# Optimization experiments

Measured on AMD Instinct MI355X. Metric: run time of the kernel, lower is better.

The kernel has to match this reference:

```python
import jax, jax.numpy as jnp
import numpy as np

H, C = 4, 128            # heads, per-head channels (GATConv(in, 128, heads=4))
HC = H * C               # 512
NEG_SLOPE = 0.2          # PyG GATConv default LeakyReLU slope
EPS_BN = 1e-5


def gat_conv(x, src, dst, W, a_src, a_dst, b, n_nodes):
    # x: [N, F_in], W: [F_in, H*C], a_src/a_dst: [H, C], b: [H*C]
    h = (x @ W).reshape(n_nodes, H, C)                       # [N,H,C]
    al_s = jnp.einsum('nhc,hc->nh', h, a_src)                # [N,H]
    al_d = jnp.einsum('nhc,hc->nh', h, a_dst)                # [N,H]
    e = jax.nn.leaky_relu(al_s[src] + al_d[dst], NEG_SLOPE)  # [E,H] per-edge logits
    m = jax.ops.segment_max(e, dst, num_segments=n_nodes)    # stable segment softmax
    p = jnp.exp(e - m[dst])
    s = jax.ops.segment_sum(p, dst, num_segments=n_nodes)
    alpha = p / (s[dst] + 1e-16)                             # [E,H]
    out = jax.ops.segment_sum(h[src] * alpha[:, :, None], dst, num_segments=n_nodes)
    return out.reshape(n_nodes, HC) + b                      # concat heads + bias


def batch_norm(x, g, b):
    mu = x.mean(0)
    var = x.var(0)  # biased, as torch BatchNorm1d uses for normalization
    return (x - mu) * jax.lax.rsqrt(var + EPS_BN) * g + b


def setup_inputs() -> dict:
    N, E, F_IN, OUT = 20000, 256000, 128, 10
    key = jax.random.key(0)
    ks = jax.random.split(key, 40)
    sc = 0.05
    inp = {
        'x': jax.random.normal(ks[0], (N, F_IN), dtype=jnp.float32),
        'edge_index': jax.random.randint(ks[1], (2, E), 0, N, dtype=jnp.int64) if jax.config.jax_enable_x64 else jax.random.randint(ks[1], (2, E), 0, N).astype(jnp.int32),
        'batch': jnp.zeros((N,), dtype=jnp.int32),
    }
    k = 2
    fin = F_IN
    for i in range(1, 5):
        inp[f'W{i}'] = jax.random.normal(ks[k], (fin, HC), dtype=jnp.float32) * sc; k += 1
        inp[f'as{i}'] = jax.random.normal(ks[k], (H, C), dtype=jnp.float32) * sc; k += 1
        inp[f'ad{i}'] = jax.random.normal(ks[k], (H, C), dtype=jnp.float32) * sc; k += 1
        inp[f'b{i}'] = jnp.zeros((HC,), dtype=jnp.float32)
        inp[f'g{i}'] = jnp.ones((HC,), dtype=jnp.float32)
        inp[f'bt{i}'] = jnp.zeros((HC,), dtype=jnp.float32)
        fin = HC
    inp['lw1'] = jax.random.normal(ks[k], (HC, 128), dtype=jnp.float32) * sc; k += 1
    inp['lb1'] = jnp.zeros((128,), dtype=jnp.float32)
    inp['lw2'] = jax.random.normal(ks[k], (128, 64), dtype=jnp.float32) * sc; k += 1
    inp['lb2'] = jnp.zeros((64,), dtype=jnp.float32)
    inp['lw3'] = jax.random.normal(ks[k], (64, OUT), dtype=jnp.float32) * sc; k += 1
    inp['lb3'] = jnp.zeros((OUT,), dtype=jnp.float32)
    return inp


def reference(x, edge_index, batch,
              W1, as1, ad1, b1, g1, bt1,
              W2, as2, ad2, b2, g2, bt2,
              W3, as3, ad3, b3, g3, bt3,
              W4, as4, ad4, b4, g4, bt4,
              lw1, lb1, lw2, lb2, lw3, lb3):
    n = x.shape[0]
    # add self-loops (PyG GATConv default add_self_loops=True)
    loops = jnp.arange(n, dtype=edge_index.dtype)
    src = jnp.concatenate([edge_index[0], loops])
    dst = jnp.concatenate([edge_index[1], loops])

    h = jax.nn.elu(gat_conv(x, src, dst, W1, as1, ad1, b1, n))
    h = batch_norm(h, g1, bt1)
    h = jax.nn.elu(gat_conv(h, src, dst, W2, as2, ad2, b2, n))
    h = batch_norm(h, g2, bt2)
    h = jax.nn.elu(gat_conv(h, src, dst, W3, as3, ad3, b3, n))
    h = batch_norm(h, g3, bt3)
    h = jax.nn.elu(gat_conv(h, src, dst, W4, as4, ad4, b4, n))
    h = batch_norm(h, g4, bt4)

    h = jax.nn.relu(h @ lw1 + lb1)   # dropout is identity in eval
    h = jax.nn.relu(h @ lw2 + lb2)
    return jax.nn.log_softmax(h @ lw3 + lb3, axis=-1)
```

## Files before the change

kernel.cpp:

```cpp
#include <hip/hip_runtime.h>
#include <hip/hip_bf16.h>
#include <math.h>

#define HC 512
#define NHEAD 4
#define NEG_SLOPE 0.2f
#define EPS_BN 1e-5f

typedef __attribute__((ext_vector_type(8))) _Float16 half8;
typedef __attribute__((ext_vector_type(4))) _Float16 half4v;
typedef __attribute__((ext_vector_type(2))) _Float16 half2v;
typedef __attribute__((ext_vector_type(4))) float f32x4;

#define GLOAD16(gptr, lptr)                                                      \
    __builtin_amdgcn_global_load_lds(                                            \
        (const __attribute__((address_space(1))) unsigned int*)(gptr),           \
        (__attribute__((address_space(3))) unsigned int*)(lptr), 16, 0, 0)

__global__ void hist_kernel(const int* __restrict__ dstE, int* __restrict__ cnt,
                            int E, int N) {
    int i = blockIdx.x * 256 + threadIdx.x;
    if (i < E + N) {
        int d = (i < E) ? dstE[i] : (i - E);
        atomicAdd(&cnt[d], 1);
    }
}

__global__ __launch_bounds__(1024) void scan_kernel(int* __restrict__ rowptr,
                                                    int* __restrict__ wr, int n) {
    __shared__ int wsum[16];
    __shared__ int carry_s;
    int t = threadIdx.x, lane = t & 63, wv = t >> 6;
    if (t == 0) carry_s = 0;
    __syncthreads();
    for (int base = 0; base < n; base += 1024) {
        int v = (base + t < n) ? rowptr[base + t] : 0;
        int x = v;
#pragma unroll
        for (int off = 1; off < 64; off <<= 1) {
            int y = __shfl_up(x, off);
            if (lane >= off) x += y;
        }
        if (lane == 63) wsum[wv] = x;
        __syncthreads();
        if (wv == 0) {
            int s = (lane < 16) ? wsum[lane] : 0;
#pragma unroll
            for (int off = 1; off < 16; off <<= 1) {
                int y = __shfl_up(s, off);
                if (lane >= off) s += y;
            }
            if (lane < 16) wsum[lane] = s;
        }
        __syncthreads();
        int woff = (wv == 0) ? 0 : wsum[wv - 1];
        int tot = wsum[15];
        int carry = carry_s;
        if (base + t < n) {
            int excl = carry + woff + x - v;
            rowptr[base + t] = excl;
            wr[base + t] = excl;
        }
        __syncthreads();
        if (t == 1023) carry_s = carry + tot;
        __syncthreads();
    }
    if (threadIdx.x == 0) rowptr[n] = carry_s;
}

__global__ void scatter_kernel(const int* __restrict__ srcE,
                               const int* __restrict__ dstE,
                               int* __restrict__ wr, int* __restrict__ csrc,
                               int E, int N) {
    int i = blockIdx.x * 256 + threadIdx.x;
    if (i < E + N) {
        int d = (i < E) ? dstE[i] : (i - E);
        int s = (i < E) ? srcE[i] : (i - E);
        int p = atomicAdd(&wr[d], 1);
        csrc[p] = s;
    }
}

__global__ __launch_bounds__(256) void advec_kernel(const double* __restrict__ stats,
                                                    const float* __restrict__ g,
                                                    const float* __restrict__ bt,
                                                    float* __restrict__ avec,
                                                    float* __restrict__ dvec,
                                                    double invN) {
    int k = blockIdx.x * 256 + threadIdx.x;
    if (k >= HC) return;
    double mu = stats[k] * invN;
    double var = stats[HC + k] * invN - mu * mu;
    float a = g[k] * (float)rsqrt(var + (double)EPS_BN);
    avec[k] = a;
    dvec[k] = bt[k] - (float)mu * a;
}

__global__ __launch_bounds__(256) void wsplit_kernel(const float* __restrict__ W,
                                                     const float* __restrict__ avec,
                                                     _Float16* __restrict__ hiT,
                                                     _Float16* __restrict__ loT,
                                                     int K, int Nc) {
    __shared__ float tile[32][33];
    int bx = blockIdx.x * 32;
    int by = blockIdx.y * 32;
    int tx = threadIdx.x & 31, ty = threadIdx.x >> 5;
#pragma unroll
    for (int r = 0; r < 32; r += 8)
        tile[ty + r][tx] = W[(size_t)(by + ty + r) * Nc + bx + tx];
    __syncthreads();
    int k = by + tx;
    float a = avec ? avec[k] : 1.f;
#pragma unroll
    for (int r = 0; r < 32; r += 8) {
        int n = bx + ty + r;
        float w = tile[tx][ty + r] * a;
        _Float16 h = (_Float16)w;
        hiT[(size_t)n * K + k] = h;
        loT[(size_t)n * K + k] = (_Float16)(w - (float)h);
    }
}

__global__ __launch_bounds__(256) void bvec_kernel(const float* __restrict__ W,
                                                   const float* __restrict__ dvec,
                                                   const float* __restrict__ extra,
                                                   float* __restrict__ bvec,
                                                   int K, int Nc) {
    int wv = (blockIdx.x * 256 + threadIdx.x) >> 6;
    int lane = threadIdx.x & 63;
    if (wv >= Nc) return;
    float s = 0.f;
    for (int k = lane; k < K; k += 64)
        s = fmaf(dvec[k], W[(size_t)k * Nc + wv], s);
#pragma unroll
    for (int off = 32; off; off >>= 1) s += __shfl_xor(s, off);
    if (lane == 0) bvec[wv] = s + (extra ? extra[wv] : 0.f);
}

__global__ __launch_bounds__(256) void xcvt_kernel(const float* __restrict__ x,
                                                   _Float16* __restrict__ xh, int total) {
    for (int i = blockIdx.x * 256 + threadIdx.x; i < total; i += gridDim.x * 256)
        xh[i] = (_Float16)x[i];
}

template <int EPI>
__global__ __launch_bounds__(256) void mfma_gemm(const _Float16* __restrict__ A,
                                                 const _Float16* __restrict__ BThi,
                                                 const _Float16* __restrict__ BTlo,
                                                 const float* __restrict__ bvec,
                                                 _Float16* __restrict__ H16,
                                                 float* __restrict__ C,
                                                 int M, int K, int Nc) {
    __shared__ _Float16 sm[3 * 4096];
    _Float16* sA  = sm;
    _Float16* sBh = sm + 4096;
    _Float16* sBl = sm + 8192;

    const int nwg = gridDim.x * gridDim.y;
    const int orig = blockIdx.y * gridDim.x + blockIdx.x;
    const int q = nwg >> 3, r = nwg & 7;
    const int xcd = orig & 7, local = orig >> 3;
    const int wgid = (xcd < r ? xcd * (q + 1) : r * (q + 1) + (xcd - r) * q) + local;
    const int bxi = wgid % gridDim.x, byi = wgid / gridDim.x;

    const int tid = threadIdx.x;
    const int wid = tid >> 6, lane = tid & 63;
    const int wm = wid >> 1, wn = wid & 1;
    const int bm = byi * 128, bn = bxi * 128;

    const int rowl = lane >> 2;
    const int cole = (lane & 3) * 8;
    const int c0 = wid * 2;

    const int frow = lane & 15;
    const int fko = (lane >> 4) * 8;

    f32x4 acc[4][4] = {};

    for (int k0 = 0; k0 < K; k0 += 32) {
#pragma unroll
        for (int cc = 0; cc < 2; ++cc) {
            int c = c0 + cc;
            int ra = bm + c * 16 + rowl; if (ra >= M) ra = M - 1;
            int rb = bn + c * 16 + rowl;
            GLOAD16(A + (size_t)ra * K + k0 + cole, &sA[c * 512]);
            GLOAD16(BThi + (size_t)rb * K + k0 + cole, &sBh[c * 512]);
            GLOAD16(BTlo + (size_t)rb * K + k0 + cole, &sBl[c * 512]);
        }
        __syncthreads();

        half8 av[4], bh[4], bl[4];
#pragma unroll
        for (int mi = 0; mi < 4; ++mi) {
            int rr = wm * 64 + mi * 16 + frow;
            av[mi] = *(const half8*)&sA[rr * 32 + fko];
        }
#pragma unroll
        for (int ni = 0; ni < 4; ++ni) {
            int rr = wn * 64 + ni * 16 + frow;
            bh[ni] = *(const half8*)&sBh[rr * 32 + fko];
            bl[ni] = *(const half8*)&sBl[rr * 32 + fko];
        }
#pragma unroll
        for (int mi = 0; mi < 4; ++mi)
#pragma unroll
            for (int ni = 0; ni < 4; ++ni) {
                acc[mi][ni] = __builtin_amdgcn_mfma_f32_16x16x32_f16(av[mi], bh[ni], acc[mi][ni], 0, 0, 0);
                acc[mi][ni] = __builtin_amdgcn_mfma_f32_16x16x32_f16(av[mi], bl[ni], acc[mi][ni], 0, 0, 0);
            }
        __syncthreads();
    }

    const int crow = (lane >> 4) * 4;
    const int ccol = lane & 15;
#pragma unroll
    for (int mi = 0; mi < 4; ++mi)
#pragma unroll
        for (int ni = 0; ni < 4; ++ni) {
            int gc = bn + wn * 64 + ni * 16 + ccol;
            float bv = bvec[gc];
#pragma unroll
            for (int rr = 0; rr < 4; ++rr) {
                int gr = bm + wm * 64 + mi * 16 + crow + rr;
                if (gr >= M) continue;
                float v = acc[mi][ni][rr] + bv;
                if (EPI == 0) {
                    H16[(size_t)gr * Nc + gc] = (_Float16)v;
                } else {
                    C[(size_t)gr * Nc + gc] = fmaxf(v, 0.f);
                }
            }
        }
}

template <int BM, int BN, int BK, int TM, int TN, int EPI>
__global__ __launch_bounds__(256) void gemm_k(const float* __restrict__ A,
                                              const float* __restrict__ B,
                                              const float* __restrict__ bias,
                                              float* __restrict__ C,
                                              int M, int K, int N) {
    constexpr int PAD = 4;
    __shared__ float sA[BK][BM + PAD];
    __shared__ float sB[BK][BN];

    const int tid = threadIdx.x;
    const int bm = blockIdx.y * BM, bn = blockIdx.x * BN;
    constexpr int TX = BN / TN;
    const int tx = tid % TX, ty = tid / TX;

    float acc[TM][TN] = {};

    constexpr int AF4 = BK / 4;
    const int a4 = tid % AF4;
    const int ar0 = tid / AF4;
    constexpr int AROWS = 256 / AF4;
    constexpr int APASS = BM / AROWS;

    constexpr int BF4 = BN / 4;
    const int b4 = tid % BF4;
    const int br0 = tid / BF4;
    constexpr int BROWS = 256 / BF4;
    constexpr int BPASS = BK / BROWS;

    for (int kt = 0; kt < K; kt += BK) {
        __syncthreads();
#pragma unroll
        for (int p = 0; p < APASS; ++p) {
            int row = ar0 + p * AROWS;
            int gr = bm + row;
            if (gr >= M) gr = M - 1;
            float4 v = *(const float4*)&A[(size_t)gr * K + kt + a4 * 4];
            sA[a4 * 4 + 0][row] = v.x;
            sA[a4 * 4 + 1][row] = v.y;
            sA[a4 * 4 + 2][row] = v.z;
            sA[a4 * 4 + 3][row] = v.w;
        }
#pragma unroll
        for (int p = 0; p < BPASS; ++p) {
            int row = br0 + p * BROWS;
            float4 v = *(const float4*)&B[(size_t)(kt + row) * N + bn + b4 * 4];
            *(float4*)&sB[row][b4 * 4] = v;
        }
        __syncthreads();
#pragma unroll
        for (int k = 0; k < BK; ++k) {
            float ar[TM], br[TN];
#pragma unroll
            for (int i = 0; i < TM; i += 4)
                *(float4*)&ar[i] = *(const float4*)&sA[k][ty * TM + i];
#pragma unroll
            for (int j = 0; j < TN; j += 4)
                *(float4*)&br[j] = *(const float4*)&sB[k][tx * TN + j];
#pragma unroll
            for (int i = 0; i < TM; ++i)
#pragma unroll
                for (int j = 0; j < TN; ++j)
                    acc[i][j] = fmaf(ar[i], br[j], acc[i][j]);
        }
    }

#pragma unroll
    for (int i = 0; i < TM; ++i) {
        int r = bm + ty * TM + i;
        if (r >= M) continue;
#pragma unroll
        for (int j = 0; j < TN; j += 4) {
            int c = bn + tx * TN + j;
            float4 v;
            v.x = acc[i][j + 0]; v.y = acc[i][j + 1];
            v.z = acc[i][j + 2]; v.w = acc[i][j + 3];
            if (EPI == 1) {
                v.x = fmaxf(v.x + bias[c + 0], 0.f);
                v.y = fmaxf(v.y + bias[c + 1], 0.f);
                v.z = fmaxf(v.z + bias[c + 2], 0.f);
                v.w = fmaxf(v.w + bias[c + 3], 0.f);
            }
            *(float4*)&C[(size_t)r * N + c] = v;
        }
    }
}

__global__ __launch_bounds__(256) void al_kernel(const _Float16* __restrict__ h16,
                                                 const float* __restrict__ asrc,
                                                 const float* __restrict__ adst,
                                                 float* __restrict__ al_s,
                                                 float* __restrict__ al_d, int N) {
    int wid = (blockIdx.x * 256 + threadIdx.x) >> 6;
    int lane = threadIdx.x & 63;
    if (wid >= N) return;
    half8 hv = *(const half8*)(h16 + (size_t)wid * HC + lane * 8);
    float ss = 0.f, sd = 0.f;
#pragma unroll
    for (int j = 0; j < 8; ++j) {
        float v = (float)hv[j];
        ss = fmaf(v, asrc[lane * 8 + j], ss);
        sd = fmaf(v, adst[lane * 8 + j], sd);
    }
#pragma unroll
    for (int off = 8; off; off >>= 1) {
        ss += __shfl_xor(ss, off);
        sd += __shfl_xor(sd, off);
    }
    if ((lane & 15) == 0) {
        al_s[wid * NHEAD + (lane >> 4)] = ss;
        al_d[wid * NHEAD + (lane >> 4)] = sd;
    }
}

__global__ __launch_bounds__(256) void attw_kernel(const float* __restrict__ al_s,
                                                   const float* __restrict__ al_d,
                                                   const int* __restrict__ rowptr,
                                                   const int* __restrict__ csrc,
                                                   float4* __restrict__ alpha, int N) {
    int node = (blockIdx.x * 256 + threadIdx.x) >> 6;
    int lane = threadIdx.x & 63;
    if (node >= N) return;
    int e0 = rowptr[node], e1 = rowptr[node + 1];
    int deg = e1 - e0;
    float4 ad4 = *(const float4*)&al_d[node * NHEAD];

    if (deg <= 64) {
        float x0 = -INFINITY, x1 = -INFINITY, x2 = -INFINITY, x3 = -INFINITY;
        if (lane < deg) {
            int s = csrc[e0 + lane];
            float4 a = *(const float4*)&al_s[s * NHEAD];
            x0 = a.x + ad4.x; x0 = (x0 > 0.f) ? x0 : NEG_SLOPE * x0;
            x1 = a.y + ad4.y; x1 = (x1 > 0.f) ? x1 : NEG_SLOPE * x1;
            x2 = a.z + ad4.z; x2 = (x2 > 0.f) ? x2 : NEG_SLOPE * x2;
            x3 = a.w + ad4.w; x3 = (x3 > 0.f) ? x3 : NEG_SLOPE * x3;
        }
        float m0 = x0, m1 = x1, m2 = x2, m3 = x3;
#pragma unroll
        for (int off = 32; off; off >>= 1) {
            m0 = fmaxf(m0, __shfl_xor(m0, off));
            m1 = fmaxf(m1, __shfl_xor(m1, off));
            m2 = fmaxf(m2, __shfl_xor(m2, off));
            m3 = fmaxf(m3, __shfl_xor(m3, off));
        }
        float p0 = (lane < deg) ? __expf(x0 - m0) : 0.f;
        float p1 = (lane < deg) ? __expf(x1 - m1) : 0.f;
        float p2 = (lane < deg) ? __expf(x2 - m2) : 0.f;
        float p3 = (lane < deg) ? __expf(x3 - m3) : 0.f;
        float s0 = p0, s1 = p1, s2 = p2, s3 = p3;
#pragma unroll
        for (int off = 32; off; off >>= 1) {
            s0 += __shfl_xor(s0, off);
            s1 += __shfl_xor(s1, off);
            s2 += __shfl_xor(s2, off);
            s3 += __shfl_xor(s3, off);
        }
        if (lane < deg) {
            float4 w;
            w.x = p0 / (s0 + 1e-16f);
            w.y = p1 / (s1 + 1e-16f);
            w.z = p2 / (s2 + 1e-16f);
            w.w = p3 / (s3 + 1e-16f);
            alpha[e0 + lane] = w;
        }
        return;
    }

    float m0 = -INFINITY, m1 = -INFINITY, m2 = -INFINITY, m3 = -INFINITY;
    for (int i = e0 + lane; i < e1; i += 64) {
        int s = csrc[i];
        float4 a = *(const float4*)&al_s[s * NHEAD];
        float e;
        e = a.x + ad4.x; e = (e > 0.f) ? e : NEG_SLOPE * e; m0 = fmaxf(m0, e);
        e = a.y + ad4.y; e = (e > 0.f) ? e : NEG_SLOPE * e; m1 = fmaxf(m1, e);
        e = a.z + ad4.z; e = (e > 0.f) ? e : NEG_SLOPE * e; m2 = fmaxf(m2, e);
        e = a.w + ad4.w; e = (e > 0.f) ? e : NEG_SLOPE * e; m3 = fmaxf(m3, e);
    }
#pragma unroll
    for (int off = 32; off; off >>= 1) {
        m0 = fmaxf(m0, __shfl_xor(m0, off));
        m1 = fmaxf(m1, __shfl_xor(m1, off));
        m2 = fmaxf(m2, __shfl_xor(m2, off));
        m3 = fmaxf(m3, __shfl_xor(m3, off));
    }
    float s0 = 0, s1 = 0, s2 = 0, s3 = 0;
    for (int i = e0 + lane; i < e1; i += 64) {
        int s = csrc[i];
        float4 a = *(const float4*)&al_s[s * NHEAD];
        float e;
        e = a.x + ad4.x; e = (e > 0.f) ? e : NEG_SLOPE * e; s0 += __expf(e - m0);
        e = a.y + ad4.y; e = (e > 0.f) ? e : NEG_SLOPE * e; s1 += __expf(e - m1);
        e = a.z + ad4.z; e = (e > 0.f) ? e : NEG_SLOPE * e; s2 += __expf(e - m2);
        e = a.w + ad4.w; e = (e > 0.f) ? e : NEG_SLOPE * e; s3 += __expf(e - m3);
    }
#pragma unroll
    for (int off = 32; off; off >>= 1) {
        s0 += __shfl_xor(s0, off);
        s1 += __shfl_xor(s1, off);
        s2 += __shfl_xor(s2, off);
        s3 += __shfl_xor(s3, off);
    }
    float r0 = 1.f / (s0 + 1e-16f), r1 = 1.f / (s1 + 1e-16f);
    float r2 = 1.f / (s2 + 1e-16f), r3 = 1.f / (s3 + 1e-16f);
    for (int i = e0 + lane; i < e1; i += 64) {
        int s = csrc[i];
        float4 a = *(const float4*)&al_s[s * NHEAD];
        float4 w;
        float e;
        e = a.x + ad4.x; e = (e > 0.f) ? e : NEG_SLOPE * e; w.x = __expf(e - m0) * r0;
        e = a.y + ad4.y; e = (e > 0.f) ? e : NEG_SLOPE * e; w.y = __expf(e - m1) * r1;
        e = a.z + ad4.z; e = (e > 0.f) ? e : NEG_SLOPE * e; w.z = __expf(e - m2) * r2;
        e = a.w + ad4.w; e = (e > 0.f) ? e : NEG_SLOPE * e; w.w = __expf(e - m3) * r3;
        alpha[i] = w;
    }
}

__global__ __launch_bounds__(256) void gath_kernel(const _Float16* __restrict__ h16,
                                                   const float4* __restrict__ alpha,
                                                   const int* __restrict__ rowptr,
                                                   const int* __restrict__ csrc,
                                                   const float* __restrict__ bias,
                                                   _Float16* __restrict__ out16, int N) {
    int gid = blockIdx.x * 256 + threadIdx.x;
    int wv = gid >> 6, lane = gid & 63;
    int node = wv >> 1, hf = wv & 1;
    if (node >= N) return;
    int e0 = rowptr[node], e1 = rowptr[node + 1];
    size_t cb = (size_t)(hf * 256 + lane * 4);
    bool hiHead = (lane & 32) != 0;

#define PICKW(q) (hf ? (hiHead ? (q).w : (q).z) : (hiHead ? (q).y : (q).x))

    float a0 = 0, a1 = 0, a2 = 0, a3 = 0;
    int i = e0;
    for (; i + 4 <= e1; i += 4) {
        int s0 = csrc[i], s1 = csrc[i + 1], s2 = csrc[i + 2], s3 = csrc[i + 3];
        float4 q0 = alpha[i], q1 = alpha[i + 1], q2 = alpha[i + 2], q3 = alpha[i + 3];
        half4v v0 = *(const half4v*)(h16 + (size_t)s0 * HC + cb);
        half4v v1 = *(const half4v*)(h16 + (size_t)s1 * HC + cb);
        half4v v2 = *(const half4v*)(h16 + (size_t)s2 * HC + cb);
        half4v v3 = *(const half4v*)(h16 + (size_t)s3 * HC + cb);
        float w0 = PICKW(q0), w1 = PICKW(q1), w2 = PICKW(q2), w3 = PICKW(q3);
        a0 = fmaf((float)v0[0], w0, a0); a1 = fmaf((float)v0[1], w0, a1);
        a2 = fmaf((float)v0[2], w0, a2); a3 = fmaf((float)v0[3], w0, a3);
        a0 = fmaf((float)v1[0], w1, a0); a1 = fmaf((float)v1[1], w1, a1);
        a2 = fmaf((float)v1[2], w1, a2); a3 = fmaf((float)v1[3], w1, a3);
        a0 = fmaf((float)v2[0], w2, a0); a1 = fmaf((float)v2[1], w2, a1);
        a2 = fmaf((float)v2[2], w2, a2); a3 = fmaf((float)v2[3], w2, a3);
        a0 = fmaf((float)v3[0], w3, a0); a1 = fmaf((float)v3[1], w3, a1);
        a2 = fmaf((float)v3[2], w3, a2); a3 = fmaf((float)v3[3], w3, a3);
    }
    for (; i < e1; ++i) {
        int s = csrc[i];
        float4 q = alpha[i];
        float w = PICKW(q);
        half4v v = *(const half4v*)(h16 + (size_t)s * HC + cb);
        a0 = fmaf((float)v[0], w, a0); a1 = fmaf((float)v[1], w, a1);
        a2 = fmaf((float)v[2], w, a2); a3 = fmaf((float)v[3], w, a3);
    }
#undef PICKW

    float4 bb = *(const float4*)&bias[cb];
    a0 += bb.x; a1 += bb.y; a2 += bb.z; a3 += bb.w;
    a0 = (a0 > 0.f) ? a0 : (__expf(a0) - 1.f);
    a1 = (a1 > 0.f) ? a1 : (__expf(a1) - 1.f);
    a2 = (a2 > 0.f) ? a2 : (__expf(a2) - 1.f);
    a3 = (a3 > 0.f) ? a3 : (__expf(a3) - 1.f);
    half4v o = {(_Float16)a0, (_Float16)a1, (_Float16)a2, (_Float16)a3};
    *(half4v*)(out16 + (size_t)node * HC + cb) = o;
}

__global__ __launch_bounds__(256) void bnstat_kernel(const _Float16* __restrict__ x,
                                                     double* __restrict__ partials,
                                                     int N) {
    __shared__ double lds[2][4][HC];
    int t = threadIdx.x;
    int lane = t & 63, wv = t >> 6;
    int c0 = lane * 8;
    const int stride = gridDim.x * 4;

    float s[8] = {}, q[8] = {};
    int r = blockIdx.x * 4 + wv;
    for (; r + stride < N; r += 2 * stride) {
        half8 v0 = *(const half8*)&x[(size_t)r * HC + c0];
        half8 v1 = *(const half8*)&x[(size_t)(r + stride) * HC + c0];
#pragma unroll
        for (int j = 0; j < 8; ++j) {
            float f0 = (float)v0[j], f1 = (float)v1[j];
            s[j] += f0 + f1;
            q[j] = fmaf(f0, f0, q[j]);
            q[j] = fmaf(f1, f1, q[j]);
        }
    }
    for (; r < N; r += stride) {
        half8 v0 = *(const half8*)&x[(size_t)r * HC + c0];
#pragma unroll
        for (int j = 0; j < 8; ++j) {
            float f0 = (float)v0[j];
            s[j] += f0;
            q[j] = fmaf(f0, f0, q[j]);
        }
    }
#pragma unroll
    for (int j = 0; j < 8; ++j) {
        lds[0][wv][c0 + j] = (double)s[j];
        lds[1][wv][c0 + j] = (double)q[j];
    }
    __syncthreads();
    if (wv == 0) {
        double* pb = partials + (size_t)blockIdx.x * 1024;
#pragma unroll
        for (int j = 0; j < 8; ++j) {
            int c = c0 + j;
            double ds = lds[0][0][c] + lds[0][1][c] + lds[0][2][c] + lds[0][3][c];
            double dq = lds[1][0][c] + lds[1][1][c] + lds[1][2][c] + lds[1][3][c];
            pb[c] = ds;
            pb[512 + c] = dq;
        }
    }
}

__global__ __launch_bounds__(256) void bnred_kernel(const double* __restrict__ partials,
                                                    double* __restrict__ stats, int nb) {
    int wv = (blockIdx.x * 256 + threadIdx.x) >> 6;
    int lane = threadIdx.x & 63;
    if (wv >= 1024) return;
    double s = 0.0;
    for (int b = lane; b < nb; b += 64)
        s += partials[(size_t)b * 1024 + wv];
#pragma unroll
    for (int off = 32; off; off >>= 1) s += __shfl_xor(s, off);
    if (lane == 0) stats[wv] = s;
}

__global__ __launch_bounds__(256) void head_kernel(const float* __restrict__ x,
                                                   const float* __restrict__ w,
                                                   const float* __restrict__ b,
                                                   float* __restrict__ out, int N) {
    int wid = (blockIdx.x * 256 + threadIdx.x) >> 6;
    int lane = threadIdx.x & 63;
    if (wid >= N) return;
    float v = x[(size_t)wid * 64 + lane];
    float my = -INFINITY;
#pragma unroll
    for (int j = 0; j < 10; ++j) {
        float t = v * w[lane * 10 + j];
#pragma unroll
        for (int off = 32; off; off >>= 1) t += __shfl_xor(t, off);
        t += b[j];
        if (lane == j) my = t;
    }
    float mx = my;
#pragma unroll
    for (int off = 32; off; off >>= 1) mx = fmaxf(mx, __shfl_xor(mx, off));
    float p = (lane < 10) ? expf(my - mx) : 0.f;
    float sum = p;
#pragma unroll
    for (int off = 32; off; off >>= 1) sum += __shfl_xor(sum, off);
    if (lane < 10) out[(size_t)wid * 10 + lane] = my - mx - logf(sum);
}

extern "C" void kernel_launch(void* const* d_in, const int* in_sizes, int n_in,
                              void* d_out, int out_size, void* d_ws, size_t ws_size,
                              hipStream_t stream) {
    const float* x = (const float*)d_in[0];
    const int* ei = (const int*)d_in[1];
    const int N = in_sizes[0] / 128;
    const int E = in_sizes[1] / 2;
    const int EN = E + N;
    const int NB_STAT = 256;

    double* stats = (double*)d_ws;
    double* partials = stats + 1024;
    float* als   = (float*)(partials + (size_t)NB_STAT * 1024);
    float* ald   = als + (size_t)N * NHEAD;
    float4* alpha = (float4*)(ald + (size_t)N * NHEAD);
    float* bvec  = (float*)(alpha + EN);
    float* avec  = bvec + 512;
    float* dvec  = avec + 512;
    float* m1    = dvec + 512;
    float* m2    = m1 + (size_t)N * 128;
    _Float16* xh   = (_Float16*)(m2 + (size_t)N * 64);
    _Float16* h16  = xh + (size_t)N * 128;
    _Float16* out16 = h16 + (size_t)N * HC;
    _Float16* wpool = out16 + (size_t)N * HC;
    _Float16* wthi[4], * wtlo[4], * wtmhi, * wtmlo;
    {
        _Float16* p = wpool;
        wthi[0] = p; p += 512 * 128;
        wtlo[0] = p; p += 512 * 128;
        for (int L = 1; L < 4; ++L) {
            wthi[L] = p; p += 512 * 512;
            wtlo[L] = p; p += 512 * 512;
        }
        wtmhi = p; p += 128 * 512;
        wtmlo = p; p += 128 * 512;
    }
    int* rowptr = (int*)(wpool + 2 * 512 * 128 + 6 * 512 * 512 + 2 * 128 * 512);
    int* wr = rowptr + (N + 1);
    int* csrc = wr + N;

    hipMemsetAsync(rowptr, 0, (N + 1) * sizeof(int), stream);
    hist_kernel<<<(EN + 255) / 256, 256, 0, stream>>>(ei + E, rowptr, E, N);
    scan_kernel<<<1, 1024, 0, stream>>>(rowptr, wr, N);
    scatter_kernel<<<(EN + 255) / 256, 256, 0, stream>>>(ei, ei + E, wr, csrc, E, N);

    wsplit_kernel<<<dim3(512 / 32, 128 / 32), 256, 0, stream>>>(
        (const float*)d_in[3], nullptr, wthi[0], wtlo[0], 128, 512);
    xcvt_kernel<<<1024, 256, 0, stream>>>(x, xh, N * 128);
    hipMemsetAsync(bvec, 0, 512 * sizeof(float), stream);

    const int nodeBlocks = (N * 64 + 255) / 256;
    const int gathBlocks = (N * 128 + 255) / 256;
    const double invN = 1.0 / (double)N;

    for (int L = 0; L < 4; ++L) {
        const float* as_ = (const float*)d_in[4 + 6 * L];
        const float* ad_ = (const float*)d_in[5 + 6 * L];
        const float* b_  = (const float*)d_in[6 + 6 * L];
        const float* g_  = (const float*)d_in[7 + 6 * L];
        const float* bt_ = (const float*)d_in[8 + 6 * L];
        const _Float16* Ain = (L == 0) ? xh : out16;
        const int curK = (L == 0) ? 128 : 512;

        mfma_gemm<0><<<dim3(HC / 128, (N + 127) / 128), 256, 0, stream>>>(
            Ain, wthi[L], wtlo[L], bvec, h16, nullptr, N, curK, HC);
        al_kernel<<<nodeBlocks, 256, 0, stream>>>(h16, as_, ad_, als, ald, N);
        attw_kernel<<<nodeBlocks, 256, 0, stream>>>(als, ald, rowptr, csrc, alpha, N);
        gath_kernel<<<gathBlocks, 256, 0, stream>>>(h16, alpha, rowptr, csrc, b_,
                                                    out16, N);
        bnstat_kernel<<<NB_STAT, 256, 0, stream>>>(out16, partials, N);
        bnred_kernel<<<256, 256, 0, stream>>>(partials, stats, NB_STAT);
        advec_kernel<<<2, 256, 0, stream>>>(stats, g_, bt_, avec, dvec, invN);

        if (L < 3) {
            const float* Wn = (const float*)d_in[3 + 6 * (L + 1)];
            wsplit_kernel<<<dim3(512 / 32, 512 / 32), 256, 0, stream>>>(
                Wn, avec, wthi[L + 1], wtlo[L + 1], 512, 512);
            bvec_kernel<<<(512 * 64 + 255) / 256, 256, 0, stream>>>(
                Wn, dvec, nullptr, bvec, 512, 512);
        } else {
            const float* lw1 = (const float*)d_in[27];
            const float* lb1 = (const float*)d_in[28];
            wsplit_kernel<<<dim3(128 / 32, 512 / 32), 256, 0, stream>>>(
                lw1, avec, wtmhi, wtmlo, 512, 128);
            bvec_kernel<<<(128 * 64 + 255) / 256, 256, 0, stream>>>(
                lw1, dvec, lb1, bvec, 512, 128);
        }
    }

    const float* lw2 = (const float*)d_in[29];
    const float* lb2 = (const float*)d_in[30];
    const float* lw3 = (const float*)d_in[31];
    const float* lb3 = (const float*)d_in[32];

    mfma_gemm<1><<<dim3(1, (N + 127) / 128), 256, 0, stream>>>(
        out16, wtmhi, wtmlo, bvec, nullptr, m1, N, 512, 128);
    gemm_k<64, 64, 16, 4, 4, 1><<<dim3(1, (N + 63) / 64), 256, 0, stream>>>(
        m1, lw2, lb2, m2, N, 128, 64);
    head_kernel<<<nodeBlocks, 256, 0, stream>>>(m2, lw3, lb3, (float*)d_out, N);
}
```

Measured before the change: 680.1 us.

## Drop split-fp16 weight correction and pad CSR rows to multiples of eight

Weights are now converted to a single fp16 copy instead of a hi/lo pair, which halves the MFMA count and the B-tile LDS traffic in every GEMM. Separately, each CSR row is padded to a multiple of eight using zeroed alpha and zeroed source indices. This lets the gather loop run a fixed 8-wide unrolled batch of loads with no remainder loop. The cost is lower weight precision, plus extra memsets and padded edges that gather node 0's features with zero weight.

Result: no change. 685.8 us (+0.8%).

```diff
diff --git a/kernel.cpp b/kernel.cpp
--- a/kernel.cpp
+++ b/kernel.cpp
@@ -9,7 +9,6 @@
 
 typedef __attribute__((ext_vector_type(8))) _Float16 half8;
 typedef __attribute__((ext_vector_type(4))) _Float16 half4v;
-typedef __attribute__((ext_vector_type(2))) _Float16 half2v;
 typedef __attribute__((ext_vector_type(4))) float f32x4;
 
 #define GLOAD16(gptr, lptr)                                                      \
@@ -27,14 +26,16 @@
 }
 
 __global__ __launch_bounds__(1024) void scan_kernel(int* __restrict__ rowptr,
-                                                    int* __restrict__ wr, int n) {
+                                                    int* __restrict__ wr,
+                                                    int* __restrict__ deg, int n) {
     __shared__ int wsum[16];
     __shared__ int carry_s;
     int t = threadIdx.x, lane = t & 63, wv = t >> 6;
     if (t == 0) carry_s = 0;
     __syncthreads();
     for (int base = 0; base < n; base += 1024) {
-        int v = (base + t < n) ? rowptr[base + t] : 0;
+        int c = (base + t < n) ? rowptr[base + t] : 0;
+        int v = (c + 7) & ~7;
         int x = v;
 #pragma unroll
         for (int off = 1; off < 64; off <<= 1) {
@@ -60,6 +61,7 @@
             int excl = carry + woff + x - v;
             rowptr[base + t] = excl;
             wr[base + t] = excl;
+            deg[base + t] = c;
         }
         __syncthreads();
         if (t == 1023) carry_s = carry + tot;
@@ -99,7 +101,6 @@
 __global__ __launch_bounds__(256) void wsplit_kernel(const float* __restrict__ W,
                                                      const float* __restrict__ avec,
                                                      _Float16* __restrict__ hiT,
-                                                     _Float16* __restrict__ loT,
                                                      int K, int Nc) {
     __shared__ float tile[32][33];
     int bx = blockIdx.x * 32;
@@ -114,10 +115,7 @@
 #pragma unroll
     for (int r = 0; r < 32; r += 8) {
         int n = bx + ty + r;
-        float w = tile[tx][ty + r] * a;
-        _Float16 h = (_Float16)w;
-        hiT[(size_t)n * K + k] = h;
-        loT[(size_t)n * K + k] = (_Float16)(w - (float)h);
+        hiT[(size_t)n * K + k] = (_Float16)(tile[tx][ty + r] * a);
     }
 }
 
@@ -145,16 +143,14 @@
 
 template <int EPI>
 __global__ __launch_bounds__(256) void mfma_gemm(const _Float16* __restrict__ A,
-                                                 const _Float16* __restrict__ BThi,
-                                                 const _Float16* __restrict__ BTlo,
+                                                 const _Float16* __restrict__ BT,
                                                  const float* __restrict__ bvec,
                                                  _Float16* __restrict__ H16,
                                                  float* __restrict__ C,
                                                  int M, int K, int Nc) {
-    __shared__ _Float16 sm[3 * 4096];
-    _Float16* sA  = sm;
-    _Float16* sBh = sm + 4096;
-    _Float16* sBl = sm + 8192;
+    __shared__ _Float16 sm[2 * 4096];
+    _Float16* sA = sm;
+    _Float16* sB = sm + 4096;
 
     const int nwg = gridDim.x * gridDim.y;
     const int orig = blockIdx.y * gridDim.x + blockIdx.x;
@@ -184,12 +180,11 @@
             int ra = bm + c * 16 + rowl; if (ra >= M) ra = M - 1;
             int rb = bn + c * 16 + rowl;
             GLOAD16(A + (size_t)ra * K + k0 + cole, &sA[c * 512]);
-            GLOAD16(BThi + (size_t)rb * K + k0 + cole, &sBh[c * 512]);
-            GLOAD16(BTlo + (size_t)rb * K + k0 + cole, &sBl[c * 512]);
-        }
-        __syncthreads();
-
-        half8 av[4], bh[4], bl[4];
+            GLOAD16(BT + (size_t)rb * K + k0 + cole, &sB[c * 512]);
+        }
+        __syncthreads();
+
+        half8 av[4], bv[4];
 #pragma unroll
         for (int mi = 0; mi < 4; ++mi) {
             int rr = wm * 64 + mi * 16 + frow;
@@ -198,16 +193,13 @@
 #pragma unroll
         for (int ni = 0; ni < 4; ++ni) {
             int rr = wn * 64 + ni * 16 + frow;
-            bh[ni] = *(const half8*)&sBh[rr * 32 + fko];
-            bl[ni] = *(const half8*)&sBl[rr * 32 + fko];
+            bv[ni] = *(const half8*)&sB[rr * 32 + fko];
         }
 #pragma unroll
         for (int mi = 0; mi < 4; ++mi)
 #pragma unroll
-            for (int ni = 0; ni < 4; ++ni) {
-                acc[mi][ni] = __builtin_amdgcn_mfma_f32_16x16x32_f16(av[mi], bh[ni], acc[mi][ni], 0, 0, 0);
-                acc[mi][ni] = __builtin_amdgcn_mfma_f32_16x16x32_f16(av[mi], bl[ni], acc[mi][ni], 0, 0, 0);
-            }
+            for (int ni = 0; ni < 4; ++ni)
+                acc[mi][ni] = __builtin_amdgcn_mfma_f32_16x16x32_f16(av[mi], bv[ni], acc[mi][ni], 0, 0, 0);
         __syncthreads();
     }
 
@@ -218,12 +210,12 @@
 #pragma unroll
         for (int ni = 0; ni < 4; ++ni) {
             int gc = bn + wn * 64 + ni * 16 + ccol;
-            float bv = bvec[gc];
+            float bvv = bvec[gc];
 #pragma unroll
             for (int rr = 0; rr < 4; ++rr) {
                 int gr = bm + wm * 64 + mi * 16 + crow + rr;
                 if (gr >= M) continue;
-                float v = acc[mi][ni][rr] + bv;
+                float v = acc[mi][ni][rr] + bvv;
                 if (EPI == 0) {
                     H16[(size_t)gr * Nc + gc] = (_Float16)v;
                 } else {
@@ -350,13 +342,15 @@
 __global__ __launch_bounds__(256) void attw_kernel(const float* __restrict__ al_s,
                                                    const float* __restrict__ al_d,
                                                    const int* __restrict__ rowptr,
+                                                   const int* __restrict__ degv,
                                                    const int* __restrict__ csrc,
                                                    float4* __restrict__ alpha, int N) {
     int node = (blockIdx.x * 256 + threadIdx.x) >> 6;
     int lane = threadIdx.x & 63;
     if (node >= N) return;
-    int e0 = rowptr[node], e1 = rowptr[node + 1];
-    int deg = e1 - e0;
+    int e0 = rowptr[node];
+    int deg = degv[node];
+    int e1 = e0 + deg;
     float4 ad4 = *(const float4*)&al_d[node * NHEAD];
 
     if (deg <= 64) {
@@ -452,6 +446,7 @@
 __global__ __launch_bounds__(256) void gath_kernel(const _Float16* __restrict__ h16,
                                                    const float4* __restrict__ alpha,
                                                    const int* __restrict__ rowptr,
+                                                   const int* __restrict__ degv,
                                                    const int* __restrict__ csrc,
                                                    const float* __restrict__ bias,
                                                    _Float16* __restrict__ out16, int N) {
@@ -459,38 +454,33 @@
     int wv = gid >> 6, lane = gid & 63;
     int node = wv >> 1, hf = wv & 1;
     if (node >= N) return;
-    int e0 = rowptr[node], e1 = rowptr[node + 1];
+    int e0 = rowptr[node];
+    int ee = e0 + ((degv[node] + 7) & ~7);
     size_t cb = (size_t)(hf * 256 + lane * 4);
     bool hiHead = (lane & 32) != 0;
 
 #define PICKW(q) (hf ? (hiHead ? (q).w : (q).z) : (hiHead ? (q).y : (q).x))
 
     float a0 = 0, a1 = 0, a2 = 0, a3 = 0;
-    int i = e0;
-    for (; i + 4 <= e1; i += 4) {
-        int s0 = csrc[i], s1 = csrc[i + 1], s2 = csrc[i + 2], s3 = csrc[i + 3];
-        float4 q0 = alpha[i], q1 = alpha[i + 1], q2 = alpha[i + 2], q3 = alpha[i + 3];
-        half4v v0 = *(const half4v*)(h16 + (size_t)s0 * HC + cb);
-        half4v v1 = *(const half4v*)(h16 + (size_t)s1 * HC + cb);
-        half4v v2 = *(const half4v*)(h16 + (size_t)s2 * HC + cb);
-        half4v v3 = *(const half4v*)(h16 + (size_t)s3 * HC + cb);
-        float w0 = PICKW(q0), w1 = PICKW(q1), w2 = PICKW(q2), w3 = PICKW(q3);
-        a0 = fmaf((float)v0[0], w0, a0); a1 = fmaf((float)v0[1], w0, a1);
-        a2 = fmaf((float)v0[2], w0, a2); a3 = fmaf((float)v0[3], w0, a3);
-        a0 = fmaf((float)v1[0], w1, a0); a1 = fmaf((float)v1[1], w1, a1);
-        a2 = fmaf((float)v1[2], w1, a2); a3 = fmaf((float)v1[3], w1, a3);
-        a0 = fmaf((float)v2[0], w2, a0); a1 = fmaf((float)v2[1], w2, a1);
-        a2 = fmaf((float)v2[2], w2, a2); a3 = fmaf((float)v2[3], w2, a3);
-        a0 = fmaf((float)v3[0], w3, a0); a1 = fmaf((float)v3[1], w3, a1);
-        a2 = fmaf((float)v3[2], w3, a2); a3 = fmaf((float)v3[3], w3, a3);
-    }
-    for (; i < e1; ++i) {
-        int s = csrc[i];
-        float4 q = alpha[i];
-        float w = PICKW(q);
-        half4v v = *(const half4v*)(h16 + (size_t)s * HC + cb);
-        a0 = fmaf((float)v[0], w, a0); a1 = fmaf((float)v[1], w, a1);
-        a2 = fmaf((float)v[2], w, a2); a3 = fmaf((float)v[3], w, a3);
+    for (int i = e0; i < ee; i += 8) {
+        int sx[8];
+        float4 qx[8];
+        half4v vx[8];
+#pragma unroll
+        for (int u = 0; u < 8; ++u) sx[u] = csrc[i + u];
+#pragma unroll
+        for (int u = 0; u < 8; ++u) qx[u] = alpha[i + u];
+#pragma unroll
+        for (int u = 0; u < 8; ++u)
+            vx[u] = *(const half4v*)(h16 + (size_t)sx[u] * HC + cb);
+#pragma unroll
+        for (int u = 0; u < 8; ++u) {
+            float w = PICKW(qx[u]);
+            a0 = fmaf((float)vx[u][0], w, a0);
+            a1 = fmaf((float)vx[u][1], w, a1);
+            a2 = fmaf((float)vx[u][2], w, a2);
+            a3 = fmaf((float)vx[u][3], w, a3);
+        }
     }
 #undef PICKW
 
@@ -546,10 +536,8 @@
 #pragma unroll
         for (int j = 0; j < 8; ++j) {
             int c = c0 + j;
-            double ds = lds[0][0][c] + lds[0][1][c] + lds[0][2][c] + lds[0][3][c];
-            double dq = lds[1][0][c] + lds[1][1][c] + lds[1][2][c] + lds[1][3][c];
-            pb[c] = ds;
-            pb[512 + c] = dq;
+            pb[c] = lds[0][0][c] + lds[0][1][c] + lds[0][2][c] + lds[0][3][c];
+            pb[512 + c] = lds[1][0][c] + lds[1][1][c] + lds[1][2][c] + lds[1][3][c];
         }
     }
 }
@@ -602,6 +590,7 @@
     const int N = in_sizes[0] / 128;
     const int E = in_sizes[1] / 2;
     const int EN = E + N;
+    const int ENP = EN + 8 * N;
     const int NB_STAT = 256;
 
     double* stats = (double*)d_ws;
@@ -609,7 +598,7 @@
     float* als   = (float*)(partials + (size_t)NB_STAT * 1024);
     float* ald   = als + (size_t)N * NHEAD;
     float4* alpha = (float4*)(ald + (size_t)N * NHEAD);
-    float* bvec  = (float*)(alpha + EN);
+    float* bvec  = (float*)(alpha + ENP);
     float* avec  = bvec + 512;
     float* dvec  = avec + 512;
     float* m1    = dvec + 512;
@@ -618,29 +607,25 @@
     _Float16* h16  = xh + (size_t)N * 128;
     _Float16* out16 = h16 + (size_t)N * HC;
     _Float16* wpool = out16 + (size_t)N * HC;
-    _Float16* wthi[4], * wtlo[4], * wtmhi, * wtmlo;
-    {
-        _Float16* p = wpool;
-        wthi[0] = p; p += 512 * 128;
-        wtlo[0] = p; p += 512 * 128;
-        for (int L = 1; L < 4; ++L) {
-            wthi[L] = p; p += 512 * 512;
-            wtlo[L] = p; p += 512 * 512;
-        }
-        wtmhi = p; p += 128 * 512;
-        wtmlo = p; p += 128 * 512;
-    }
-    int* rowptr = (int*)(wpool + 2 * 512 * 128 + 6 * 512 * 512 + 2 * 128 * 512);
+    _Float16* wthi[4], * wtmhi;
+    _Float16* p = wpool;
+    wthi[0] = p; p += 512 * 128;
+    for (int L = 1; L < 4; ++L) { wthi[L] = p; p += 512 * 512; }
+    wtmhi = p; p += 128 * 512;
+    int* rowptr = (int*)p;
     int* wr = rowptr + (N + 1);
-    int* csrc = wr + N;
+    int* degv = wr + N;
+    int* csrc = degv + N;
 
     hipMemsetAsync(rowptr, 0, (N + 1) * sizeof(int), stream);
+    hipMemsetAsync(csrc, 0, (size_t)ENP * sizeof(int), stream);
+    hipMemsetAsync(alpha, 0, (size_t)ENP * sizeof(float4), stream);
     hist_kernel<<<(EN + 255) / 256, 256, 0, stream>>>(ei + E, rowptr, E, N);
-    scan_kernel<<<1, 1024, 0, stream>>>(rowptr, wr, N);
+    scan_kernel<<<1, 1024, 0, stream>>>(rowptr, wr, degv, N);
     scatter_kernel<<<(EN + 255) / 256, 256, 0, stream>>>(ei, ei + E, wr, csrc, E, N);
 
     wsplit_kernel<<<dim3(512 / 32, 128 / 32), 256, 0, stream>>>(
-        (const float*)d_in[3], nullptr, wthi[0], wtlo[0], 128, 512);
+        (const float*)d_in[3], nullptr, wthi[0], 128, 512);
     xcvt_kernel<<<1024, 256, 0, stream>>>(x, xh, N * 128);
     hipMemsetAsync(bvec, 0, 512 * sizeof(float), stream);
 
@@ -658,11 +643,12 @@
         const int curK = (L == 0) ? 128 : 512;
 
         mfma_gemm<0><<<dim3(HC / 128, (N + 127) / 128), 256, 0, stream>>>(
-            Ain, wthi[L], wtlo[L], bvec, h16, nullptr, N, curK, HC);
+            Ain, wthi[L], bvec, h16, nullptr, N, curK, HC);
         al_kernel<<<nodeBlocks, 256, 0, stream>>>(h16, as_, ad_, als, ald, N);
-        attw_kernel<<<nodeBlocks, 256, 0, stream>>>(als, ald, rowptr, csrc, alpha, N);
-        gath_kernel<<<gathBlocks, 256, 0, stream>>>(h16, alpha, rowptr, csrc, b_,
-                                                    out16, N);
+        attw_kernel<<<nodeBlocks, 256, 0, stream>>>(als, ald, rowptr, degv, csrc,
+                                                    alpha, N);
+        gath_kernel<<<gathBlocks, 256, 0, stream>>>(h16, alpha, rowptr, degv, csrc,
+                                                    b_, out16, N);
         bnstat_kernel<<<NB_STAT, 256, 0, stream>>>(out16, partials, N);
         bnred_kernel<<<256, 256, 0, stream>>>(partials, stats, NB_STAT);
         advec_kernel<<<2, 256, 0, stream>>>(stats, g_, bt_, avec, dvec, invN);
@@ -670,14 +656,14 @@
         if (L < 3) {
             const float* Wn = (const float*)d_in[3 + 6 * (L + 1)];
             wsplit_kernel<<<dim3(512 / 32, 512 / 32), 256, 0, stream>>>(
-                Wn, avec, wthi[L + 1], wtlo[L + 1], 512, 512);
+                Wn, avec, wthi[L + 1], 512, 512);
             bvec_kernel<<<(512 * 64 + 255) / 256, 256, 0, stream>>>(
                 Wn, dvec, nullptr, bvec, 512, 512);
         } else {
             const float* lw1 = (const float*)d_in[27];
             const float* lb1 = (const float*)d_in[28];
             wsplit_kernel<<<dim3(128 / 32, 512 / 32), 256, 0, stream>>>(
-                lw1, avec, wtmhi, wtmlo, 512, 128);
+                lw1, avec, wtmhi, 512, 128);
             bvec_kernel<<<(128 * 64 + 255) / 256, 256, 0, stream>>>(
                 lw1, dvec, lb1, bvec, 512, 128);
         }
@@ -689,7 +675,7 @@
     const float* lb3 = (const float*)d_in[32];
 
     mfma_gemm<1><<<dim3(1, (N + 127) / 128), 256, 0, stream>>>(
-        out16, wtmhi, wtmlo, bvec, nullptr, m1, N, 512, 128);
+        out16, wtmhi, bvec, nullptr, m1, N, 512, 128);
     gemm_k<64, 64, 16, 4, 4, 1><<<dim3(1, (N + 63) / 64), 256, 0, stream>>>(
         m1, lw2, lb2, m2, N, 128, 64);
     head_kernel<<<nodeBlocks, 256, 0, stream>>>(m2, lw3, lb3, (float*)d_out, N);
```
